# Kernel tuning notes

Measured on AMD Instinct MI355X. Metric: run time of the kernel, lower is better.

## Reference

```python
import jax, jax.numpy as jnp
import numpy as np

B, S, H = 4, 512, 768
D, M = 24, 96          # hdim_proj_dim, hdim_mlp_hidden
O = 2 * max(128, H // 2)  # val_mlp hidden = 768


def setup_inputs() -> dict:
    key = jax.random.key(0)
    ks = jax.random.split(key, 14)
    u = lambda k, shp, fan_in: jax.random.uniform(k, shp, jnp.float32, -1.0, 1.0) / np.float32(np.sqrt(fan_in))
    return {
        'H_j': jax.random.normal(ks[0], (B, S, H), jnp.float32),
        'H_i': jax.random.normal(ks[1], (B, S, H), jnp.float32),
        'Wpj': u(ks[2], (H, D), H),
        'Wpi': u(ks[3], (H, D), H),
        'Ws1': u(ks[4], (4 * D, M), 4 * D),
        'bs1': u(ks[5], (M,), 4 * D),
        'ws2': u(ks[6], (M,), M),
        'bs2': u(ks[7], (), M),
        'Wv1': u(ks[8], (3 * H, O), 3 * H),
        'bv1': u(ks[9], (O,), 3 * H),
        'Wv2': u(ks[10], (O, H), O),
        'bv2': u(ks[11], (H,), O),
        'alpha': jnp.float32(0.05),
        'attn_mask': jnp.ones((B, S), jnp.int32),
    }


def reference(H_j, H_i, Wpj, Wpi, Ws1, bs1, ws2, bs2, Wv1, bv1, Wv2, bv2, alpha, attn_mask):
    # Projections [B,S,D]
    Zj = H_j @ Wpj
    Zi = H_i @ Wpi
    # 4term score MLP, first layer decomposed over the concat blocks:
    # cat(Zj_p, Zi_p, Zj_p*Zi_p, |Zj_p - Zi_p|) @ Ws1
    W1j, W1i, W1h, W1d = Ws1[:D], Ws1[D:2 * D], Ws1[2 * D:3 * D], Ws1[3 * D:]
    tj = Zj @ W1j                                   # [B,P,M]
    ti = Zi @ W1i                                   # [B,Q,M]
    th = jnp.einsum('bpd,bqd,dm->bpqm', Zj, Zi, W1h)  # hadamard term
    diff = jnp.abs(Zj[:, :, None, :] - Zi[:, None, :, :])  # [B,P,Q,D]
    td = jnp.einsum('bpqd,dm->bpqm', diff, W1d)
    hid = jax.nn.relu(tj[:, :, None, :] + ti[:, None, :, :] + th + td + bs1)  # [B,P,Q,M]
    logits = jnp.einsum('bpqm,m->bpq', hid, ws2) + bs2  # [B,P,Q]
    # mask over source tokens (last dim); token_temp == 1.0 so no division
    mask = attn_mask.astype(logits.dtype)
    logits = logits + (1.0 - mask)[:, None, :] * jnp.finfo(logits.dtype).min
    probs = jax.nn.softmax(logits, axis=-1)
    ctx = jnp.einsum('bpq,bqh->bph', probs, H_i)    # [B,S,H]
    # val_mlp on cat(ctx, H_j, ctx*H_j), first layer decomposed
    Wc, Wj, Wh = Wv1[:H], Wv1[H:2 * H], Wv1[2 * H:]
    mhid = jax.nn.relu(ctx @ Wc + H_j @ Wj + (ctx * H_j) @ Wh + bv1)
    msg = mhid @ Wv2 + bv2
    # dropout is identity in eval mode
    return alpha * msg
```

## Files before the change

kernel.cpp:

```cpp
#include <hip/hip_runtime.h>
#include <hip/hip_bf16.h>

#define Bb 4
#define Ss 512
#define Hh 768
#define Dd 24
#define Mm 96
#define Oo 768

typedef __bf16 bf16x8 __attribute__((ext_vector_type(8)));
typedef float f32x4 __attribute__((ext_vector_type(4)));

__device__ __forceinline__ void transpose_tile(
    const float* __restrict__ s, __bf16* __restrict__ d,
    int R, int C, int bx, int by, float* smem, int tid)
{
    const int x = tid & 31, y = tid >> 5;
    const int c0 = bx * 32, r0 = by * 32;
    #pragma unroll
    for (int i = 0; i < 4; ++i)
        smem[(y + 8 * i) * 33 + x] = s[(size_t)(r0 + y + 8 * i) * C + c0 + x];
    __syncthreads();
    #pragma unroll
    for (int i = 0; i < 4; ++i)
        d[(size_t)(c0 + y + 8 * i) * R + r0 + x] = (__bf16)smem[x * 33 + (y + 8 * i)];
}

__global__ __launch_bounds__(256) void prep_kernel(
    const float* __restrict__ Hj, const float* __restrict__ Hi,
    const float* __restrict__ Wpj, const float* __restrict__ Wpi,
    const float* __restrict__ Wv1, const float* __restrict__ Wv2,
    float* __restrict__ Zj, float* __restrict__ Zi,
    __bf16* __restrict__ HiT, __bf16* __restrict__ Wv1T,
    __bf16* __restrict__ Wv2T, __bf16* __restrict__ Acat)
{
    __shared__ float smem[1088];
    const int bid = blockIdx.x;
    const int tid = threadIdx.x;

    if (bid < 4096) {
        const int row = bid & 2047;
        const int which = bid >> 11;
        const float* src = (which ? Hi : Hj) + (size_t)row * Hh;
        const float* W = which ? Wpi : Wpj;
        float* Z = which ? Zi : Zj;
        float* rowbuf = smem;
        float* partial = smem + 768;
        for (int i = tid; i < Hh; i += 256) rowbuf[i] = src[i];
        __syncthreads();
        if (tid < 192) {
            const int d = tid % Dd;
            const int c = tid / Dd;
            const int h0 = c * 96;
            float s = 0.f;
            #pragma unroll 4
            for (int h = h0; h < h0 + 96; ++h) s = fmaf(rowbuf[h], W[h * Dd + d], s);
            partial[c * Dd + d] = s;
        }
        __syncthreads();
        if (tid < Dd) {
            float s = 0.f;
            #pragma unroll
            for (int c = 0; c < 8; ++c) s += partial[c * Dd + tid];
            Z[(size_t)row * Dd + tid] = s;
        }
    } else if (bid < 5632) {
        int rem = bid - 4096;
        const int bz = rem / 384; rem %= 384;
        transpose_tile(Hi + (size_t)bz * Ss * Hh, HiT + (size_t)bz * Hh * Ss,
                       Ss, Hh, rem % 24, rem / 24, smem, tid);
    } else if (bid < 7360) {
        const int rem = bid - 5632;
        transpose_tile(Wv1, Wv1T, 3 * Hh, Oo, rem % 24, rem / 24, smem, tid);
    } else if (bid < 7936) {
        const int rem = bid - 7360;
        transpose_tile(Wv2, Wv2T, Oo, Hh, rem % 24, rem / 24, smem, tid);
    } else {
        const int idx = (bid - 7936) * 256 + tid;
        const int row = idx / 96, c8 = idx % 96;
        const float* s = Hj + (size_t)row * Hh + c8 * 8;
        const float4 u = *(const float4*)s;
        const float4 v = *(const float4*)(s + 4);
        bf16x8 o;
        o[0]=(__bf16)u.x; o[1]=(__bf16)u.y; o[2]=(__bf16)u.z; o[3]=(__bf16)u.w;
        o[4]=(__bf16)v.x; o[5]=(__bf16)v.y; o[6]=(__bf16)v.z; o[7]=(__bf16)v.w;
        *(bf16x8*)&Acat[(size_t)row * 2304 + Hh + c8 * 8] = o;
    }
}

__global__ __launch_bounds__(256) void pair_kernel(
    const float* __restrict__ Zj, const float* __restrict__ Zi,
    const float* __restrict__ Ws1, const float* __restrict__ bs1,
    const float* __restrict__ ws2, const float* __restrict__ bs2p,
    const int* __restrict__ mask, __bf16* __restrict__ probs)
{
    const int bp = blockIdx.x;
    const int b  = bp >> 9;
    const int tid  = threadIdx.x;
    const int lane = tid & 63;
    const int wid  = tid >> 6;
    const int col  = lane & 15;
    const int g    = lane >> 4;

    __shared__ float zjall[Dd];
    __shared__ float rowadd[Mm];
    __shared__ float logitsl[Ss];
    __shared__ float red[8];

    if (tid < Dd) zjall[tid] = Zj[(size_t)bp * Dd + tid];
    __syncthreads();
    if (tid < Mm) {
        float s = bs1[tid];
        #pragma unroll
        for (int d = 0; d < Dd; ++d) s = fmaf(zjall[d], Ws1[d * Mm + tid], s);
        rowadd[tid] = s;
    }
    __syncthreads();

    float zj8[8];
    if (g < 3) {
        const float* zr = Zj + (size_t)bp * Dd + g * 8;
        const float4 u = *(const float4*)zr;
        const float4 v = *(const float4*)(zr + 4);
        zj8[0]=u.x; zj8[1]=u.y; zj8[2]=u.z; zj8[3]=u.w;
        zj8[4]=v.x; zj8[5]=v.y; zj8[6]=v.z; zj8[7]=v.w;
    } else {
        #pragma unroll
        for (int j = 0; j < 8; ++j) zj8[j] = 0.f;
    }

    bf16x8 bw[6][2];
    float ws2r[6];
    #pragma unroll
    for (int n = 0; n < 6; ++n) {
        const int m = n * 16 + col;
        ws2r[n] = ws2[m];
        bf16x8 b0, b1;
        if (g < 3) {
            #pragma unroll
            for (int j = 0; j < 8; ++j) {
                const int d = g * 8 + j;
                b0[j] = (__bf16)(fmaf(zj8[j], Ws1[(2 * Dd + d) * Mm + m],
                                      Ws1[(Dd + d) * Mm + m]));
                b1[j] = (__bf16)(Ws1[(3 * Dd + d) * Mm + m]);
            }
        } else {
            #pragma unroll
            for (int j = 0; j < 8; ++j) { b0[j] = (__bf16)0.f; b1[j] = (__bf16)0.f; }
            b0[0] = (__bf16)rowadd[m];
        }
        bw[n][0] = b0; bw[n][1] = b1;
    }

    const float* zib = Zi + (size_t)b * Ss * Dd;

    #pragma unroll 2
    for (int t = 0; t < 8; ++t) {
        const int q0 = wid * 128 + t * 16;
        bf16x8 a0, a1;
        if (g < 3) {
            const float* zr = zib + (size_t)(q0 + col) * Dd + g * 8;
            const float4 u = *(const float4*)zr;
            const float4 v = *(const float4*)(zr + 4);
            a0[0]=(__bf16)u.x; a0[1]=(__bf16)u.y; a0[2]=(__bf16)u.z; a0[3]=(__bf16)u.w;
            a0[4]=(__bf16)v.x; a0[5]=(__bf16)v.y; a0[6]=(__bf16)v.z; a0[7]=(__bf16)v.w;
            a1[0]=(__bf16)fabsf(zj8[0]-u.x); a1[1]=(__bf16)fabsf(zj8[1]-u.y);
            a1[2]=(__bf16)fabsf(zj8[2]-u.z); a1[3]=(__bf16)fabsf(zj8[3]-u.w);
            a1[4]=(__bf16)fabsf(zj8[4]-v.x); a1[5]=(__bf16)fabsf(zj8[5]-v.y);
            a1[6]=(__bf16)fabsf(zj8[6]-v.z); a1[7]=(__bf16)fabsf(zj8[7]-v.w);
        } else {
            #pragma unroll
            for (int j = 0; j < 8; ++j) { a0[j] = (__bf16)0.f; a1[j] = (__bf16)0.f; }
            a0[0] = (__bf16)1.0f;
        }

        f32x4 acc[6];
        #pragma unroll
        for (int n = 0; n < 6; ++n) acc[n] = (f32x4){0.f, 0.f, 0.f, 0.f};
        #pragma unroll
        for (int n = 0; n < 6; ++n) {
            acc[n] = __builtin_amdgcn_mfma_f32_16x16x32_bf16(a0, bw[n][0], acc[n], 0, 0, 0);
            acc[n] = __builtin_amdgcn_mfma_f32_16x16x32_bf16(a1, bw[n][1], acc[n], 0, 0, 0);
        }

        float lsum[4] = {0.f, 0.f, 0.f, 0.f};
        #pragma unroll
        for (int n = 0; n < 6; ++n)
            #pragma unroll
            for (int r = 0; r < 4; ++r)
                lsum[r] = fmaf(fmaxf(acc[n][r], 0.f), ws2r[n], lsum[r]);
        #pragma unroll
        for (int off = 1; off <= 8; off <<= 1) {
            #pragma unroll
            for (int r = 0; r < 4; ++r) lsum[r] += __shfl_xor(lsum[r], off);
        }
        if (col == 0) {
            float4 o = {lsum[0], lsum[1], lsum[2], lsum[3]};
            *(float4*)&logitsl[q0 + g * 4] = o;
        }
    }
    __syncthreads();

    const float bs2v = bs2p[0];
    const int* mrow = mask + (size_t)b * Ss;
    float l0 = logitsl[tid]       + bs2v + (1.0f - (float)mrow[tid])       * (-3.402823466e+38f);
    float l1 = logitsl[tid + 256] + bs2v + (1.0f - (float)mrow[tid + 256]) * (-3.402823466e+38f);
    float vmax = fmaxf(l0, l1);
    #pragma unroll
    for (int off = 32; off > 0; off >>= 1) vmax = fmaxf(vmax, __shfl_xor(vmax, off));
    if (lane == 0) red[wid] = vmax;
    __syncthreads();
    const float mx = fmaxf(fmaxf(red[0], red[1]), fmaxf(red[2], red[3]));
    const float e0 = __expf(l0 - mx);
    const float e1 = __expf(l1 - mx);
    float vs = e0 + e1;
    #pragma unroll
    for (int off = 32; off > 0; off >>= 1) vs += __shfl_xor(vs, off);
    if (lane == 0) red[4 + wid] = vs;
    __syncthreads();
    const float inv = 1.0f / (red[4] + red[5] + red[6] + red[7]);
    __bf16* prow = probs + (size_t)bp * Ss;
    prow[tid] = (__bf16)(e0 * inv);
    prow[tid + 256] = (__bf16)(e1 * inv);
}

template<int MODE>
__global__ __launch_bounds__(256) void gemm_kernel(
    const __bf16* __restrict__ A, const __bf16* __restrict__ Bt,
    const float* __restrict__ Hjf, const float* __restrict__ bias,
    const float* __restrict__ alphap,
    __bf16* __restrict__ obf, float* __restrict__ of)
{
    constexpr int K = (MODE == 0) ? 512 : (MODE == 1) ? 2304 : 768;
    constexpr int NIT = K / 64;
    constexpr int LDT = 72;

    __shared__ __bf16 As[64 * LDT];
    __shared__ __bf16 Bs[64 * LDT];

    const int tid = threadIdx.x;
    const int lane = tid & 63;
    const int wid = tid >> 6;
    const int col = lane & 15, g = lane >> 4;
    const int wm = wid >> 1, wn = wid & 1;
    const int r0 = blockIdx.x * 64;
    const int n0 = blockIdx.y * 64;
    const __bf16* Btb = (MODE == 0) ? Bt + (size_t)(r0 >> 9) * (Hh * Ss) : Bt;

    const int srow = tid >> 2;
    const int sc8  = (tid & 3) * 16;
    const __bf16* ag = A   + (size_t)(r0 + srow) * K + sc8;
    const __bf16* bg = Btb + (size_t)(n0 + srow) * K + sc8;
    __bf16* asl = &As[srow * LDT + sc8];
    __bf16* bsl = &Bs[srow * LDT + sc8];

    bf16x8 ra0 = *(const bf16x8*)(ag);
    bf16x8 ra1 = *(const bf16x8*)(ag + 8);
    bf16x8 rb0 = *(const bf16x8*)(bg);
    bf16x8 rb1 = *(const bf16x8*)(bg + 8);

    f32x4 acc[2][2];
    #pragma unroll
    for (int mi = 0; mi < 2; ++mi)
        #pragma unroll
        for (int ni = 0; ni < 2; ++ni) acc[mi][ni] = (f32x4){0.f, 0.f, 0.f, 0.f};

    for (int it = 0; it < NIT; ++it) {
        __syncthreads();
        *(bf16x8*)(asl)     = ra0;
        *(bf16x8*)(asl + 8) = ra1;
        *(bf16x8*)(bsl)     = rb0;
        *(bf16x8*)(bsl + 8) = rb1;
        __syncthreads();
        if (it + 1 < NIT) {
            const int kk = (it + 1) * 64;
            ra0 = *(const bf16x8*)(ag + kk);
            ra1 = *(const bf16x8*)(ag + kk + 8);
            rb0 = *(const bf16x8*)(bg + kk);
            rb1 = *(const bf16x8*)(bg + kk + 8);
        }
        #pragma unroll
        for (int h = 0; h < 2; ++h) {
            bf16x8 a0 = *(const bf16x8*)&As[(wm * 32 + col)      * LDT + h * 32 + g * 8];
            bf16x8 a1 = *(const bf16x8*)&As[(wm * 32 + 16 + col) * LDT + h * 32 + g * 8];
            bf16x8 b0 = *(const bf16x8*)&Bs[(wn * 32 + col)      * LDT + h * 32 + g * 8];
            bf16x8 b1 = *(const bf16x8*)&Bs[(wn * 32 + 16 + col) * LDT + h * 32 + g * 8];
            acc[0][0] = __builtin_amdgcn_mfma_f32_16x16x32_bf16(a0, b0, acc[0][0], 0, 0, 0);
            acc[0][1] = __builtin_amdgcn_mfma_f32_16x16x32_bf16(a0, b1, acc[0][1], 0, 0, 0);
            acc[1][0] = __builtin_amdgcn_mfma_f32_16x16x32_bf16(a1, b0, acc[1][0], 0, 0, 0);
            acc[1][1] = __builtin_amdgcn_mfma_f32_16x16x32_bf16(a1, b1, acc[1][1], 0, 0, 0);
        }
    }

    const float al = (MODE == 2) ? alphap[0] : 0.f;
    #pragma unroll
    for (int mi = 0; mi < 2; ++mi) {
        #pragma unroll
        for (int r = 0; r < 4; ++r) {
            const int row = r0 + wm * 32 + mi * 16 + g * 4 + r;
            #pragma unroll
            for (int ni = 0; ni < 2; ++ni) {
                const int cn = n0 + wn * 32 + ni * 16 + col;
                const float v = acc[mi][ni][r];
                if (MODE == 0) {
                    const float hjv = Hjf[(size_t)row * Hh + cn];
                    obf[(size_t)row * 2304 + cn] = (__bf16)v;
                    obf[(size_t)row * 2304 + 1536 + cn] = (__bf16)(v * hjv);
                } else if (MODE == 1) {
                    obf[(size_t)row * Oo + cn] = (__bf16)fmaxf(v + bias[cn], 0.f);
                } else {
                    of[(size_t)row * Hh + cn] = al * (v + bias[cn]);
                }
            }
        }
    }
}

extern "C" void kernel_launch(void* const* d_in, const int* in_sizes, int n_in,
                              void* d_out, int out_size, void* d_ws, size_t ws_size,
                              hipStream_t stream)
{
    const float* Hj  = (const float*)d_in[0];
    const float* Hi  = (const float*)d_in[1];
    const float* Wpj = (const float*)d_in[2];
    const float* Wpi = (const float*)d_in[3];
    const float* Ws1 = (const float*)d_in[4];
    const float* bs1 = (const float*)d_in[5];
    const float* ws2 = (const float*)d_in[6];
    const float* bs2 = (const float*)d_in[7];
    const float* Wv1 = (const float*)d_in[8];
    const float* bv1 = (const float*)d_in[9];
    const float* Wv2 = (const float*)d_in[10];
    const float* bv2 = (const float*)d_in[11];
    const float* alpha = (const float*)d_in[12];
    const int* mask  = (const int*)d_in[13];

    float* ws = (float*)d_ws;
    float* Zj      = ws;
    float* Zi      = Zj + 49152;
    float* probs_f = Zi + 49152;
    float* HiT_f   = probs_f + 524288;
    float* Wv2T_f  = HiT_f + 786432;
    float* mhid_f  = Wv2T_f + 294912;
    float* Acat_f  = mhid_f + 786432;
    float* Wv1T_f  = Acat_f + 2359296;

    __bf16* probs_bf = (__bf16*)probs_f;
    __bf16* HiT      = (__bf16*)HiT_f;
    __bf16* Wv2T     = (__bf16*)Wv2T_f;
    __bf16* mhid_bf  = (__bf16*)mhid_f;
    __bf16* Acat     = (__bf16*)Acat_f;
    __bf16* Wv1T     = (__bf16*)Wv1T_f;

    prep_kernel<<<dim3(8704), 256, 0, stream>>>(
        Hj, Hi, Wpj, Wpi, Wv1, Wv2, Zj, Zi, HiT, Wv1T, Wv2T, Acat);
    pair_kernel<<<dim3(Bb * Ss), 256, 0, stream>>>(
        Zj, Zi, Ws1, bs1, ws2, bs2, mask, probs_bf);
    gemm_kernel<0><<<dim3(2048 / 64, Hh / 64), 256, 0, stream>>>(
        probs_bf, HiT, Hj, nullptr, nullptr, Acat, nullptr);
    gemm_kernel<1><<<dim3(2048 / 64, Oo / 64), 256, 0, stream>>>(
        Acat, Wv1T, nullptr, bv1, nullptr, mhid_bf, nullptr);
    gemm_kernel<2><<<dim3(2048 / 64, Hh / 64), 256, 0, stream>>>(
        mhid_bf, Wv2T, nullptr, bv2, alpha, nullptr, (float*)d_out);
}
```

Baseline: 180.7 us.

## Precompute per-row score MLP weights in a separate kernel and swap MFMA operand roles

Adds a wprep kernel that builds, for each query row, the bf16 weight fragments: the Zj-dependent hadamard fold, the row bias term, and the diff weights. It uses a transposed copy of Ws1 made in the prep kernel. Zi is now stored padded to 32 columns with a constant 1 in column 24, so the row bias comes in through the padded K slot. The pair kernel then loads ready fragments, swaps the A/B roles of the MFMA so the reduction over the hidden dimension needs fewer shuffles, and prefetches the next Zi tile. This removes scattered Ws1 reads and the per-block serial setup, at the cost of an extra launch and a roughly 25 MB Bw buffer written and read back.

Result: slower. 211.6 us (+17.1%).

```diff
diff --git a/kernel.cpp b/kernel.cpp
--- a/kernel.cpp
+++ b/kernel.cpp
@@ -30,7 +30,8 @@
     const float* __restrict__ Hj, const float* __restrict__ Hi,
     const float* __restrict__ Wpj, const float* __restrict__ Wpi,
     const float* __restrict__ Wv1, const float* __restrict__ Wv2,
-    float* __restrict__ Zj, float* __restrict__ Zi,
+    const float* __restrict__ Ws1,
+    float* __restrict__ Zj, float* __restrict__ Zip, float* __restrict__ WsT,
     __bf16* __restrict__ HiT, __bf16* __restrict__ Wv1T,
     __bf16* __restrict__ Wv2T, __bf16* __restrict__ Acat)
 {
@@ -43,7 +44,6 @@
         const int which = bid >> 11;
         const float* src = (which ? Hi : Hj) + (size_t)row * Hh;
         const float* W = which ? Wpi : Wpj;
-        float* Z = which ? Zi : Zj;
         float* rowbuf = smem;
         float* partial = smem + 768;
         for (int i = tid; i < Hh; i += 256) rowbuf[i] = src[i];
@@ -62,8 +62,11 @@
             float s = 0.f;
             #pragma unroll
             for (int c = 0; c < 8; ++c) s += partial[c * Dd + tid];
-            Z[(size_t)row * Dd + tid] = s;
-        }
+            if (which) Zip[(size_t)row * 32 + tid] = s;
+            else       Zj[(size_t)row * Dd + tid] = s;
+        }
+        if (which && tid >= Dd && tid < 32)
+            Zip[(size_t)row * 32 + tid] = (tid == 24) ? 1.0f : 0.0f;
     } else if (bid < 5632) {
         int rem = bid - 4096;
         const int bz = rem / 384; rem %= 384;
@@ -75,7 +78,7 @@
     } else if (bid < 7936) {
         const int rem = bid - 7360;
         transpose_tile(Wv2, Wv2T, Oo, Hh, rem % 24, rem / 24, smem, tid);
-    } else {
+    } else if (bid < 8704) {
         const int idx = (bid - 7936) * 256 + tid;
         const int row = idx / 96, c8 = idx % 96;
         const float* s = Hj + (size_t)row * Hh + c8 * 8;
@@ -85,14 +88,58 @@
         o[0]=(__bf16)u.x; o[1]=(__bf16)u.y; o[2]=(__bf16)u.z; o[3]=(__bf16)u.w;
         o[4]=(__bf16)v.x; o[5]=(__bf16)v.y; o[6]=(__bf16)v.z; o[7]=(__bf16)v.w;
         *(bf16x8*)&Acat[(size_t)row * 2304 + Hh + c8 * 8] = o;
+    } else {
+        __shared__ float W[96 * 97];
+        for (int i = tid; i < 96 * 96; i += 256) W[(i / 96) * 97 + (i % 96)] = Ws1[i];
+        __syncthreads();
+        for (int i = tid; i < 96 * 96; i += 256) WsT[i] = W[(i % 96) * 97 + (i / 96)];
+    }
+}
+
+__global__ __launch_bounds__(256) void wprep_kernel(
+    const float* __restrict__ Zj, const float* __restrict__ WsT,
+    const float* __restrict__ bs1, __bf16* __restrict__ Bw)
+{
+    const int p = blockIdx.x;
+    const int tid = threadIdx.x;
+    __shared__ float zj[Dd];
+    if (tid < Dd) zj[tid] = Zj[(size_t)p * Dd + tid];
+    __syncthreads();
+    #pragma unroll
+    for (int i = tid; i < 768; i += 256) {
+        const int m = i >> 3, k8 = i & 7;
+        const int k0 = k8 * 8;
+        const float* wr = WsT + (size_t)m * 96;
+        bf16x8 o;
+        if (k8 < 3) {
+            #pragma unroll
+            for (int j = 0; j < 8; ++j) {
+                const int k = k0 + j;
+                o[j] = (__bf16)fmaf(zj[k], wr[48 + k], wr[24 + k]);
+            }
+        } else if (k8 == 3) {
+            float tj = bs1[m];
+            #pragma unroll
+            for (int d = 0; d < Dd; ++d) tj = fmaf(zj[d], wr[d], tj);
+            o[0] = (__bf16)tj;
+            #pragma unroll
+            for (int j = 1; j < 8; ++j) o[j] = (__bf16)0.f;
+        } else if (k8 < 7) {
+            #pragma unroll
+            for (int j = 0; j < 8; ++j) o[j] = (__bf16)wr[72 + (k0 - 32) + j];
+        } else {
+            #pragma unroll
+            for (int j = 0; j < 8; ++j) o[j] = (__bf16)0.f;
+        }
+        *(bf16x8*)(Bw + (((size_t)p * 96 + m) << 6) + k0) = o;
     }
 }
 
 __global__ __launch_bounds__(256) void pair_kernel(
-    const float* __restrict__ Zj, const float* __restrict__ Zi,
-    const float* __restrict__ Ws1, const float* __restrict__ bs1,
-    const float* __restrict__ ws2, const float* __restrict__ bs2p,
-    const int* __restrict__ mask, __bf16* __restrict__ probs)
+    const float* __restrict__ Zj, const float* __restrict__ Zip,
+    const __bf16* __restrict__ Bw, const float* __restrict__ ws2,
+    const float* __restrict__ bs2p, const int* __restrict__ mask,
+    __bf16* __restrict__ probs)
 {
     const int bp = blockIdx.x;
     const int b  = bp >> 9;
@@ -102,20 +149,22 @@
     const int col  = lane & 15;
     const int g    = lane >> 4;
 
-    __shared__ float zjall[Dd];
-    __shared__ float rowadd[Mm];
     __shared__ float logitsl[Ss];
     __shared__ float red[8];
 
-    if (tid < Dd) zjall[tid] = Zj[(size_t)bp * Dd + tid];
-    __syncthreads();
-    if (tid < Mm) {
-        float s = bs1[tid];
-        #pragma unroll
-        for (int d = 0; d < Dd; ++d) s = fmaf(zjall[d], Ws1[d * Mm + tid], s);
-        rowadd[tid] = s;
-    }
-    __syncthreads();
+    bf16x8 aw[6][2];
+    #pragma unroll
+    for (int n = 0; n < 6; ++n) {
+        const __bf16* base = Bw + (((size_t)bp * 96 + n * 16 + col) << 6) + g * 8;
+        aw[n][0] = *(const bf16x8*)(base);
+        aw[n][1] = *(const bf16x8*)(base + 32);
+    }
+    float ws2r[6][4];
+    #pragma unroll
+    for (int n = 0; n < 6; ++n) {
+        const float4 w4 = *(const float4*)&ws2[n * 16 + g * 4];
+        ws2r[n][0] = w4.x; ws2r[n][1] = w4.y; ws2r[n][2] = w4.z; ws2r[n][3] = w4.w;
+    }
 
     float zj8[8];
     if (g < 3) {
@@ -129,75 +178,43 @@
         for (int j = 0; j < 8; ++j) zj8[j] = 0.f;
     }
 
-    bf16x8 bw[6][2];
-    float ws2r[6];
-    #pragma unroll
-    for (int n = 0; n < 6; ++n) {
-        const int m = n * 16 + col;
-        ws2r[n] = ws2[m];
+    const float* zb = Zip + ((size_t)(b * Ss + wid * 128 + col) * 32) + g * 8;
+
+    float4 cu = *(const float4*)zb;
+    float4 cv = *(const float4*)(zb + 4);
+
+    for (int t = 0; t < 8; ++t) {
+        const float4 u = cu, v = cv;
+        if (t + 1 < 8) {
+            const float* zr = zb + (size_t)(t + 1) * 16 * 32;
+            cu = *(const float4*)zr; cv = *(const float4*)(zr + 4);
+        }
         bf16x8 b0, b1;
-        if (g < 3) {
-            #pragma unroll
-            for (int j = 0; j < 8; ++j) {
-                const int d = g * 8 + j;
-                b0[j] = (__bf16)(fmaf(zj8[j], Ws1[(2 * Dd + d) * Mm + m],
-                                      Ws1[(Dd + d) * Mm + m]));
-                b1[j] = (__bf16)(Ws1[(3 * Dd + d) * Mm + m]);
-            }
-        } else {
-            #pragma unroll
-            for (int j = 0; j < 8; ++j) { b0[j] = (__bf16)0.f; b1[j] = (__bf16)0.f; }
-            b0[0] = (__bf16)rowadd[m];
-        }
-        bw[n][0] = b0; bw[n][1] = b1;
-    }
-
-    const float* zib = Zi + (size_t)b * Ss * Dd;
-
-    #pragma unroll 2
-    for (int t = 0; t < 8; ++t) {
-        const int q0 = wid * 128 + t * 16;
-        bf16x8 a0, a1;
-        if (g < 3) {
-            const float* zr = zib + (size_t)(q0 + col) * Dd + g * 8;
-            const float4 u = *(const float4*)zr;
-            const float4 v = *(const float4*)(zr + 4);
-            a0[0]=(__bf16)u.x; a0[1]=(__bf16)u.y; a0[2]=(__bf16)u.z; a0[3]=(__bf16)u.w;
-            a0[4]=(__bf16)v.x; a0[5]=(__bf16)v.y; a0[6]=(__bf16)v.z; a0[7]=(__bf16)v.w;
-            a1[0]=(__bf16)fabsf(zj8[0]-u.x); a1[1]=(__bf16)fabsf(zj8[1]-u.y);
-            a1[2]=(__bf16)fabsf(zj8[2]-u.z); a1[3]=(__bf16)fabsf(zj8[3]-u.w);
-            a1[4]=(__bf16)fabsf(zj8[4]-v.x); a1[5]=(__bf16)fabsf(zj8[5]-v.y);
-            a1[6]=(__bf16)fabsf(zj8[6]-v.z); a1[7]=(__bf16)fabsf(zj8[7]-v.w);
-        } else {
-            #pragma unroll
-            for (int j = 0; j < 8; ++j) { a0[j] = (__bf16)0.f; a1[j] = (__bf16)0.f; }
-            a0[0] = (__bf16)1.0f;
-        }
+        b0[0]=(__bf16)u.x; b0[1]=(__bf16)u.y; b0[2]=(__bf16)u.z; b0[3]=(__bf16)u.w;
+        b0[4]=(__bf16)v.x; b0[5]=(__bf16)v.y; b0[6]=(__bf16)v.z; b0[7]=(__bf16)v.w;
+        b1[0]=(__bf16)fabsf(zj8[0]-u.x); b1[1]=(__bf16)fabsf(zj8[1]-u.y);
+        b1[2]=(__bf16)fabsf(zj8[2]-u.z); b1[3]=(__bf16)fabsf(zj8[3]-u.w);
+        b1[4]=(__bf16)fabsf(zj8[4]-v.x); b1[5]=(__bf16)fabsf(zj8[5]-v.y);
+        b1[6]=(__bf16)fabsf(zj8[6]-v.z); b1[7]=(__bf16)fabsf(zj8[7]-v.w);
 
         f32x4 acc[6];
         #pragma unroll
         for (int n = 0; n < 6; ++n) acc[n] = (f32x4){0.f, 0.f, 0.f, 0.f};
         #pragma unroll
         for (int n = 0; n < 6; ++n) {
-            acc[n] = __builtin_amdgcn_mfma_f32_16x16x32_bf16(a0, bw[n][0], acc[n], 0, 0, 0);
-            acc[n] = __builtin_amdgcn_mfma_f32_16x16x32_bf16(a1, bw[n][1], acc[n], 0, 0, 0);
-        }
-
-        float lsum[4] = {0.f, 0.f, 0.f, 0.f};
+            acc[n] = __builtin_amdgcn_mfma_f32_16x16x32_bf16(aw[n][0], b0, acc[n], 0, 0, 0);
+            acc[n] = __builtin_amdgcn_mfma_f32_16x16x32_bf16(aw[n][1], b1, acc[n], 0, 0, 0);
+        }
+
+        float lsum = 0.f;
         #pragma unroll
         for (int n = 0; n < 6; ++n)
             #pragma unroll
             for (int r = 0; r < 4; ++r)
-                lsum[r] = fmaf(fmaxf(acc[n][r], 0.f), ws2r[n], lsum[r]);
-        #pragma unroll
-        for (int off = 1; off <= 8; off <<= 1) {
-            #pragma unroll
-            for (int r = 0; r < 4; ++r) lsum[r] += __shfl_xor(lsum[r], off);
-        }
-        if (col == 0) {
-            float4 o = {lsum[0], lsum[1], lsum[2], lsum[3]};
-            *(float4*)&logitsl[q0 + g * 4] = o;
-        }
+                lsum = fmaf(fmaxf(acc[n][r], 0.f), ws2r[n][r], lsum);
+        lsum += __shfl_xor(lsum, 16);
+        lsum += __shfl_xor(lsum, 32);
+        if (lane < 16) logitsl[wid * 128 + t * 16 + lane] = lsum;
     }
     __syncthreads();
 
@@ -337,13 +354,15 @@
 
     float* ws = (float*)d_ws;
     float* Zj      = ws;
-    float* Zi      = Zj + 49152;
-    float* probs_f = Zi + 49152;
+    float* Zip     = Zj + 49152;
+    float* WsT     = Zip + 65536;
+    float* probs_f = WsT + 9216;
     float* HiT_f   = probs_f + 524288;
     float* Wv2T_f  = HiT_f + 786432;
     float* mhid_f  = Wv2T_f + 294912;
     float* Acat_f  = mhid_f + 786432;
     float* Wv1T_f  = Acat_f + 2359296;
+    float* Bw_f    = Wv1T_f + 884736;
 
     __bf16* probs_bf = (__bf16*)probs_f;
     __bf16* HiT      = (__bf16*)HiT_f;
@@ -351,11 +370,13 @@
     __bf16* mhid_bf  = (__bf16*)mhid_f;
     __bf16* Acat     = (__bf16*)Acat_f;
     __bf16* Wv1T     = (__bf16*)Wv1T_f;
-
-    prep_kernel<<<dim3(8704), 256, 0, stream>>>(
-        Hj, Hi, Wpj, Wpi, Wv1, Wv2, Zj, Zi, HiT, Wv1T, Wv2T, Acat);
+    __bf16* Bw       = (__bf16*)Bw_f;
+
+    prep_kernel<<<dim3(8705), 256, 0, stream>>>(
+        Hj, Hi, Wpj, Wpi, Wv1, Wv2, Ws1, Zj, Zip, WsT, HiT, Wv1T, Wv2T, Acat);
+    wprep_kernel<<<dim3(2048), 256, 0, stream>>>(Zj, WsT, bs1, Bw);
     pair_kernel<<<dim3(Bb * Ss), 256, 0, stream>>>(
-        Zj, Zi, Ws1, bs1, ws2, bs2, mask, probs_bf);
+        Zj, Zip, Bw, ws2, bs2, mask, probs_bf);
     gemm_kernel<0><<<dim3(2048 / 64, Hh / 64), 256, 0, stream>>>(
         probs_bf, HiT, Hj, nullptr, nullptr, Acat, nullptr);
     gemm_kernel<1><<<dim3(2048 / 64, Oo / 64), 256, 0, stream>>>(
```
